# Kernel tuning notes

Hardware: AMD Instinct MI355X
Metric: run time of the kernel (lower is better)

## Reference

```python
import jax, jax.numpy as jnp
from jax import lax
import numpy as np

BLOCKS = 6
DIM = 768
D_STATE = 16
D_CONV = 4
EXPAND = 2
HEADDIM = 64
D_INNER = EXPAND * DIM              # 1536
NHEADS = D_INNER // HEADDIM        # 24
CONV_DIM = D_INNER + 2 * D_STATE   # 1568 (ngroups=1)
D_IN_PROJ = 2 * D_INNER + 2 * D_STATE + NHEADS  # 3128
NPITCH = 128


def setup_inputs() -> dict:
    key = jax.random.key(0)
    ks = jax.random.split(key, 16)
    B, L = 4, 4096
    s = 0.02
    return {
        "x": jax.random.normal(ks[0], (B, L, DIM), jnp.float32),
        "type_IDs": jax.random.randint(ks[1], (B, L), 0, 2),
        "in_proj_w": jax.random.normal(ks[2], (BLOCKS, D_IN_PROJ, DIM), jnp.float32) * s,
        "conv_w": jax.random.normal(ks[3], (BLOCKS, CONV_DIM, D_CONV), jnp.float32) * 0.1,
        "conv_b": jnp.zeros((BLOCKS, CONV_DIM), jnp.float32),
        "dt_bias": jax.random.uniform(ks[4], (BLOCKS, NHEADS), jnp.float32, -4.0, -2.0),
        "A_log": jnp.tile(jnp.log(jnp.linspace(1.0, 16.0, NHEADS, dtype=jnp.float32)), (BLOCKS, 1)),
        "D": jnp.ones((BLOCKS, NHEADS), jnp.float32),
        "norm_w": jnp.ones((BLOCKS, D_INNER), jnp.float32),
        "out_proj_w": jax.random.normal(ks[5], (BLOCKS, DIM, D_INNER), jnp.float32) * s,
        "head_w": jax.random.normal(ks[6], (2, DIM, DIM), jnp.float32) * s,
        "head_b": jnp.zeros((2, DIM), jnp.float32),
        "head_out_w": jax.random.normal(ks[7], (2, 4, NPITCH, DIM), jnp.float32) * s,
        "head_out_b": jnp.zeros((2, 4, NPITCH), jnp.float32),
    }


def _mamba2_block(x, Wi, cw, cb, dtb, Alog, Dp, nw, Wo):
    B, L, _ = x.shape
    zxbcdt = jnp.einsum('bld,ed->ble', x, Wi)                 # [B,L,D_IN_PROJ]
    z = zxbcdt[..., :D_INNER]
    xBC = zxbcdt[..., D_INNER:D_INNER + CONV_DIM]
    dt = zxbcdt[..., -NHEADS:]
    # causal depthwise conv1d over time
    xc = jnp.pad(jnp.swapaxes(xBC, 1, 2), ((0, 0), (0, 0), (D_CONV - 1, 0)))
    xBC = lax.conv_general_dilated(xc, cw[:, None, :], (1,), 'VALID',
                                   feature_group_count=CONV_DIM,
                                   dimension_numbers=('NCH', 'OIH', 'NCH'))
    xBC = jax.nn.silu(jnp.swapaxes(xBC, 1, 2) + cb)            # [B,L,CONV_DIM]
    xs = xBC[..., :D_INNER].reshape(B, L, NHEADS, HEADDIM)
    Bm = xBC[..., D_INNER:D_INNER + D_STATE]                   # [B,L,N]
    Cm = xBC[..., D_INNER + D_STATE:]                          # [B,L,N]
    dt = jax.nn.softplus(dt + dtb)                             # [B,L,H]
    dA = jnp.exp(dt * (-jnp.exp(Alog)))                        # [B,L,H]
    dtx = dt[..., None] * xs                                   # [B,L,H,P]

    def step(h, inp):
        dA_t, dtx_t, B_t, C_t = inp
        h = h * dA_t[:, :, None, None] + dtx_t[..., None] * B_t[:, None, None, :]
        y = jnp.einsum('bhpn,bn->bhp', h, C_t)
        return h, y

    h0 = jnp.zeros((B, NHEADS, HEADDIM, D_STATE), x.dtype)
    mv = lambda a: jnp.moveaxis(a, 1, 0)
    _, ys = lax.scan(step, h0, (mv(dA), mv(dtx), mv(Bm), mv(Cm)))
    y = jnp.moveaxis(ys, 0, 1) + Dp[None, None, :, None] * xs   # [B,L,H,P]
    y = y.reshape(B, L, D_INNER) * jax.nn.silu(z)               # gated
    y = y * lax.rsqrt(jnp.mean(y * y, -1, keepdims=True) + 1e-5) * nw
    return jnp.einsum('bli,di->bld', y, Wo)


def _head(t, hw, hb, ow, ob):
    h = jnp.einsum('bld,ed->ble', t, hw) + hb
    velocity = jnp.einsum('bld,pd->blp', h, ow[0]) + ob[0]
    onset = jax.nn.sigmoid(jnp.einsum('bld,pd->blp', h, ow[1]) + ob[1])
    offset = jax.nn.sigmoid(jnp.einsum('bld,pd->blp', h, ow[2]) + ob[2])
    frames = jax.nn.sigmoid(jnp.einsum('bld,pd->blp', h, ow[3]) + ob[3])
    return velocity, frames, onset, offset


def reference(x, type_IDs, in_proj_w, conv_w, conv_b, dt_bias, A_log, D,
              norm_w, out_proj_w, head_w, head_b, head_out_w, head_out_b):
    for i in range(BLOCKS):
        x = _mamba2_block(x, in_proj_w[i], conv_w[i], conv_b[i], dt_bias[i],
                          A_log[i], D[i], norm_w[i], out_proj_w[i])
    cmask = (type_IDs == 0).astype(x.dtype)[..., None]
    fmask = (type_IDs == 1).astype(x.dtype)[..., None]
    cv, cf, con, coff = _head(x, head_w[0], head_b[0], head_out_w[0], head_out_b[0])
    fv, ff, fon, foff = _head(x, head_w[1], head_b[1], head_out_w[1], head_out_b[1])
    # masked (instead of ragged boolean gather) to stay jit-compatible
    return jnp.stack([cv * cmask, cf * cmask, con * cmask, coff * cmask,
                      fv * fmask, ff * fmask, fon * fmask, foff * fmask])
```

## Files before the change

### kernel.cpp

```cpp
#include <hip/hip_runtime.h>
#include <cstdint>
#include <cstddef>

#define L_SEQ   4096
#define BATCH   4
#define DIMM    768
#define D_INNER 1536
#define NHEADS  24
#define HEADDIM 64
#define D_STATE 16
#define CONVD   1568
#define D_IPROJ 3128
#define ZXP     3200
#define SEGLEN  64
#define NSEG    (L_SEQ / SEGLEN)
#define BCP     44

typedef _Float16 f16x8 __attribute__((ext_vector_type(8)));
typedef _Float16 f16x4 __attribute__((ext_vector_type(4)));
typedef float    f32x4 __attribute__((ext_vector_type(4)));

__device__ __forceinline__ void glds16(const _Float16* g, _Float16* l) {
  __builtin_amdgcn_global_load_lds(
      (__attribute__((address_space(1))) unsigned int*)g,
      (__attribute__((address_space(3))) unsigned int*)l, 16, 0, 0);
}

__device__ __forceinline__ float fsilu(float x) {
  return x * __builtin_amdgcn_rcpf(1.f + __expf(-x));
}
__device__ __forceinline__ float fsig(float x) {
  return __builtin_amdgcn_rcpf(1.f + __expf(-x));
}

template <int OM>
__global__ __launch_bounds__(512, 1) void gemm256(
    const _Float16* __restrict__ A, long lda,
    const _Float16* __restrict__ W,
    const float* __restrict__ bias,
    _Float16* __restrict__ C, long ldc,
    int M, int N, int K)
{
  __shared__ __align__(16) _Float16 lds[65536];
  const int tid = threadIdx.x;
  const int lane = tid & 63, wid = tid >> 6;
  const int wm = wid >> 2, wn = wid & 3;
  const int la = lane & 15, lg = lane >> 4;
  const int srow = lane >> 3, schunk = lane & 7;

  const int nbx = gridDim.x, nby = gridDim.y;
  const int flat = blockIdx.y * nbx + blockIdx.x;
  const int xcd = flat & 7, idx = flat >> 3;
  const int rpx = nby >> 3;
  const long m0 = (long)(xcd * rpx + idx % rpx) * 256;
  const int n0 = (idx / rpx) * 256;

  const int nkt = K >> 6;

  auto stage = [&](int buf, int ht, int kt) {
#pragma unroll
    for (int p = 0; p < 2; ++p) {
      int rg = wid * 2 + p;
      int rl = (ht & 1) * 128 + rg * 8 + srow;
      int scn = schunk ^ (rl & 7);
      const _Float16* src;
      if (ht < 2) {
        src = A + (m0 + rl) * lda + kt * 64 + scn * 8;
      } else {
        int n = n0 + rl; if (n >= N) n = N - 1;
        src = W + (long)n * (long)K + kt * 64 + scn * 8;
      }
      _Float16* dst = lds + (ht >= 2 ? 32768 : 0) + buf * 16384
                          + ((ht & 1) * 128 + rg * 8) * 64;
      glds16(src, dst);
    }
  };

  f32x4 acc[8][4] = {};

  stage(0, 0, 0); stage(0, 1, 0); stage(0, 2, 0); stage(0, 3, 0);
  asm volatile("s_waitcnt vmcnt(0)" ::: "memory");
  __syncthreads();

  int buf = 0;
  for (int kt = 0; kt < nkt; ++kt) {
    const bool nl = (kt + 1 < nkt);
    const _Float16* Ab = lds + buf * 16384;
    const _Float16* Bb = lds + 32768 + buf * 16384;
    f16x8 bfr[4][2];
#pragma unroll
    for (int ph = 0; ph < 4; ++ph) {
      if (nl) stage(buf ^ 1, ph, kt + 1);
      if (ph == 0) {
#pragma unroll
        for (int j = 0; j < 4; ++j)
#pragma unroll
          for (int ks = 0; ks < 2; ++ks) {
            int rb = wn * 64 + j * 16 + la;
            int cc = ks * 4 + lg;
            bfr[j][ks] = *(const f16x8*)&Bb[rb * 64 + ((cc ^ (rb & 7)) << 3)];
          }
      }
      f16x8 af[2][2];
#pragma unroll
      for (int ii = 0; ii < 2; ++ii)
#pragma unroll
        for (int ks = 0; ks < 2; ++ks) {
          int ra = wm * 128 + (ph * 2 + ii) * 16 + la;
          int cc = ks * 4 + lg;
          af[ii][ks] = *(const f16x8*)&Ab[ra * 64 + ((cc ^ (ra & 7)) << 3)];
        }
      __builtin_amdgcn_s_setprio(1);
#pragma unroll
      for (int ii = 0; ii < 2; ++ii)
#pragma unroll
        for (int j = 0; j < 4; ++j)
#pragma unroll
          for (int ks = 0; ks < 2; ++ks)
            acc[ph * 2 + ii][j] = __builtin_amdgcn_mfma_f32_16x16x32_f16(
                af[ii][ks], bfr[j][ks], acc[ph * 2 + ii][j], 0, 0, 0);
      __builtin_amdgcn_s_setprio(0);
      if (ph == 3 && nl) asm volatile("s_waitcnt vmcnt(0)" ::: "memory");
      __syncthreads();
    }
    buf ^= 1;
  }

  _Float16* ep = lds + wid * 8192;
#pragma unroll
  for (int i = 0; i < 8; ++i)
#pragma unroll
    for (int j = 0; j < 4; ++j) {
      float bs = 0.f;
      if (OM == 2) bs = bias[n0 + wn * 64 + j * 16 + la];
#pragma unroll
      for (int r = 0; r < 4; ++r) {
        int row = i * 16 + lg * 4 + r;
        int jj = j ^ (row & 3);
        ep[row * 64 + jj * 16 + la] = (_Float16)(acc[i][j][r] + bs);
      }
    }
  asm volatile("s_waitcnt lgkmcnt(0)" ::: "memory");
#pragma unroll
  for (int it = 0; it < 16; ++it) {
    int row = it * 8 + (lane >> 3);
    int hc = lane & 7;
    int jj = (hc >> 1) ^ (row & 3);
    f16x8 v = *(const f16x8*)&ep[row * 64 + jj * 16 + (hc & 1) * 8];
    int gcol = n0 + wn * 64 + hc * 8;
    long grow = m0 + wm * 128 + row;
    if (gcol < N)
      *(f16x8*)&C[grow * ldc + gcol] = v;
  }
}

template <int OM>
__global__ __launch_bounds__(256, 2) void gemm_mfma(
    const _Float16* __restrict__ A, int lda,
    const _Float16* __restrict__ W,
    const float* __restrict__ bias,
    void* __restrict__ Cv, long ldc, long extra,
    int M, int N, int K,
    const int* __restrict__ tidsp, int thead)
{
  __shared__ __align__(16) char smem[33792];
  _Float16* As = (_Float16*)smem;
  _Float16* Ws = (_Float16*)(smem + 16384);
  const int tid = threadIdx.x;
  const int lane = tid & 63, wid = tid >> 6;
  const int wr = wid >> 1, wc = wid & 1;

  const int nbx = gridDim.x, nby = gridDim.y;
  const int flat = blockIdx.y * nbx + blockIdx.x;
  const int xcd = flat & 7;
  const int bidx = flat >> 3;
  const int rpx = nby >> 3;
  const int rl = bidx % rpx;
  const int ct = bidx / rpx;
  const long m0 = (long)(xcd * rpx + rl) * 128;
  const int n0 = ct * 128;

  const int la = lane & 15, lg = lane >> 4;
  const int srow = lane >> 3, schunk = lane & 7;

  f32x4 acc[4][4] = {};

  for (int k0 = 0; k0 < K; k0 += 64) {
    __syncthreads();
#pragma unroll
    for (int p = 0; p < 4; ++p) {
      const int rg = (wid << 2) + p;
      const int row = (rg << 3) + srow;
      const int scn = schunk ^ (row & 7);
      glds16(A + (m0 + row) * (long)lda + k0 + scn * 8, As + rg * 512);
      int n = n0 + row; if (n >= N) n = N - 1;
      glds16(W + (long)n * K + k0 + scn * 8, Ws + rg * 512);
    }
    asm volatile("s_waitcnt vmcnt(0)" ::: "memory");
    __syncthreads();
#pragma unroll
    for (int ks = 0; ks < 2; ++ks) {
      const int cc = ks * 4 + lg;
      f16x8 af[4], bfr[4];
#pragma unroll
      for (int i = 0; i < 4; ++i) {
        int ra = wr * 64 + i * 16 + la;
        int rb = wc * 64 + i * 16 + la;
        af[i]  = *(const f16x8*)&As[ra * 64 + ((cc ^ (ra & 7)) << 3)];
        bfr[i] = *(const f16x8*)&Ws[rb * 64 + ((cc ^ (rb & 7)) << 3)];
      }
#pragma unroll
      for (int i = 0; i < 4; ++i)
#pragma unroll
        for (int j = 0; j < 4; ++j)
          acc[i][j] = __builtin_amdgcn_mfma_f32_16x16x32_f16(af[i], bfr[j], acc[i][j], 0, 0, 0);
    }
  }

  float* epi = (float*)smem;
#pragma unroll
  for (int ph = 0; ph < 2; ++ph) {
    __syncthreads();
    if (wr == ph) {
#pragma unroll
      for (int i = 0; i < 4; ++i)
#pragma unroll
        for (int j = 0; j < 4; ++j)
#pragma unroll
          for (int r = 0; r < 4; ++r)
            epi[(i * 16 + lg * 4 + r) * 132 + wc * 64 + j * 16 + la] = acc[i][j][r];
    }
    __syncthreads();
    if (OM == 3) {
      const int q = n0 >> 7;
      const int rr = tid >> 5;
      const int ch = tid & 31;
#pragma unroll
      for (int ps = 0; ps < 8; ++ps) {
        int lrow = ps * 8 + rr;
        long gr = m0 + ph * 64 + lrow;
        float keep = (tidsp[gr] == thead) ? 1.f : 0.f;
        float4 v = *(float4*)&epi[lrow * 132 + ch * 4];
        float o[4] = {v.x, v.y, v.z, v.w};
#pragma unroll
        for (int e = 0; e < 4; ++e) {
          float vv = o[e] + bias[n0 + ch * 4 + e];
          if (q != 0) vv = fsig(vv);
          o[e] = vv * keep;
        }
        *(float4*)((float*)Cv + (long)q * extra + gr * 128 + ch * 4) =
            make_float4(o[0], o[1], o[2], o[3]);
      }
    }
  }
}

__global__ __launch_bounds__(256) void cvt_kernel(
    const float* __restrict__ src, _Float16* __restrict__ dst, long n4)
{
  long i = (long)blockIdx.x * 256 + threadIdx.x;
  long stride = (long)gridDim.x * 256;
  for (; i < n4; i += stride) {
    float4 v = *(const float4*)(src + i * 4);
    f16x4 o = { (_Float16)v.x, (_Float16)v.y, (_Float16)v.z, (_Float16)v.w };
    *(f16x4*)(dst + i * 4) = o;
  }
}

__global__ __launch_bounds__(256) void pack_head_kernel(
    const float* __restrict__ how, const float* __restrict__ hob,
    _Float16* __restrict__ howb, float* __restrict__ hobp)
{
  const int wmap[4] = {0, 3, 1, 2};
  int idx = blockIdx.x * 256 + threadIdx.x;
  if (idx < 2 * 512 * 768) {
    int t = idx / (512 * 768);
    int rem = idx - t * 512 * 768;
    int q = rem / (128 * 768);
    int rem2 = rem - q * 128 * 768;
    howb[idx] = (_Float16)how[((size_t)(t * 4 + wmap[q])) * 128 * 768 + rem2];
  }
  if (idx < 1024) {
    int t = idx >> 9, rem = idx & 511;
    int q = rem >> 7, pp = rem & 127;
    hobp[idx] = hob[(t * 4 + wmap[q]) * 128 + pp];
  }
}

__global__ __launch_bounds__(64) void ssdA_kernel(
    const _Float16* __restrict__ zx, const float* __restrict__ cw,
    const float* __restrict__ cb, const float* __restrict__ dtb,
    const float* __restrict__ alog, const float* __restrict__ Dv,
    _Float16* __restrict__ ybuf, _Float16* __restrict__ bcbuf,
    float* __restrict__ Hseg, float* __restrict__ cumq)
{
  __shared__ __align__(16) char sm[14848];
  _Float16* XV    = (_Float16*)sm;
  _Float16* bcraw = (_Float16*)sm;
  _Float16* BC    = (_Float16*)(sm + 8448);
  float* sa  = (float*)(sm + 14080);
  float* sdt = (float*)(sm + 14336);
  float* sws = (float*)(sm + 14592);
  const int lane = threadIdx.x;
  const int seg = blockIdx.x & (NSEG - 1);
  const int bh = blockIdx.x >> 6;
  const int h = bh % NHEADS, b = bh / NHEADS;
  const int bl0 = b * L_SEQ + seg * SEGLEN;
  const float LOG2E = 1.44269504088896f;

  for (int i = lane; i < 67 * 4; i += 64) {
    int r = i >> 2, q = (i & 3) << 3;
    f16x8 v = {};
    if (seg > 0 || r >= 3)
      v = *(const f16x8*)&zx[(size_t)(bl0 - 3 + r) * ZXP + 2 * D_INNER + q];
    *(f16x8*)&bcraw[r * 32 + q] = v;
  }
  {
    float raw = (float)zx[(size_t)(bl0 + lane) * ZXP + (D_INNER + CONVD) + h] + dtb[h];
    float sp = (raw > 20.f) ? raw : log1pf(__expf(raw));
    sdt[lane] = sp;
    float av = __expf(alog[h]) * sp * LOG2E;
#pragma unroll
    for (int off = 1; off < 64; off <<= 1) {
      float tv = __shfl_up(av, off, 64);
      if (lane >= off) av += tv;
    }
    sa[lane] = av;
    cumq[(size_t)bh * L_SEQ + seg * SEGLEN + lane] = exp2f(-av);
    float alast = __shfl(av, 63, 64);
    sws[lane] = exp2f(av - alast) * sp;
  }
  __syncthreads();

  for (int i = lane; i < SEGLEN * 32; i += 64) {
    int t = i >> 5, c = i & 31;
    float acc = cb[D_INNER + c];
#pragma unroll
    for (int k = 0; k < 4; ++k)
      acc = fmaf(cw[(D_INNER + c) * 4 + k], (float)bcraw[(t + k) * 32 + c], acc);
    _Float16 sh = (_Float16)fsilu(acc);
    BC[t * BCP + c] = sh;
    bcbuf[(size_t)(bl0 + t) * 32 + c] = sh;
  }
  __syncthreads();

  const int xch = h * HEADDIM + lane;
  const _Float16* xg = zx + (size_t)bl0 * ZXP + D_INNER + xch;
  const float cwx0 = cw[xch * 4 + 0], cwx1 = cw[xch * 4 + 1];
  const float cwx2 = cw[xch * 4 + 2], cwx3 = cw[xch * 4 + 3];
  const float cbx = cb[xch];
  float xw0 = 0.f, xw1 = 0.f, xw2 = 0.f;
  if (seg > 0) {
    xw0 = (float)xg[-3 * (long)ZXP];
    xw1 = (float)xg[-2 * (long)ZXP];
    xw2 = (float)xg[-1 * (long)ZXP];
  }
  float xcur = (float)xg[0];
  for (int t = 0; t < SEGLEN; ++t) {
    float xnext = (t < SEGLEN - 1) ? (float)xg[(size_t)(t + 1) * ZXP] : 0.f;
    float xa = cbx;
    xa = fmaf(cwx0, xw0, xa);
    xa = fmaf(cwx1, xw1, xa);
    xa = fmaf(cwx2, xw2, xa);
    xa = fmaf(cwx3, xcur, xa);
    XV[t * 66 + lane] = (_Float16)fsilu(xa);
    xw0 = xw1; xw1 = xw2; xw2 = xcur; xcur = xnext;
  }
  __syncthreads();

  const int la = lane & 15, lg = lane >> 4;

  f16x4 Mfrag[4][4];
  {
    f16x4 cf[4];
    float sat[4];
#pragma unroll
    for (int tt = 0; tt < 4; ++tt) {
      cf[tt] = *(const f16x4*)&BC[(tt * 16 + la) * BCP + 16 + lg * 4];
      sat[tt] = sa[tt * 16 + la];
    }
#pragma unroll
    for (int st = 0; st < 4; ++st) {
      f16x4 bfA = *(const f16x4*)&BC[(st * 16 + la) * BCP + lg * 4];
#pragma unroll
      for (int tt = 0; tt < 4; ++tt) {
        f32x4 a1 = {};
        a1 = __builtin_amdgcn_mfma_f32_16x16x16f16(bfA, cf[tt], a1, 0, 0, 0);
        f16x4 m;
#pragma unroll
        for (int r = 0; r < 4; ++r) {
          int s = st * 16 + lg * 4 + r;
          int t = tt * 16 + la;
          float mv = 0.f;
          if (s <= t) mv = a1[r] * exp2f(sa[s] - sat[tt]);
          m[r] = (_Float16)mv;
        }
        Mfrag[st][tt] = m;
      }
    }
  }

  f16x4 b3[4];
#pragma unroll
  for (int st = 0; st < 4; ++st) {
    f16x4 v;
#pragma unroll
    for (int e = 0; e < 4; ++e)
      v[e] = BC[(st * 16 + lg * 4 + e) * BCP + la];
    b3[st] = v;
  }

  const float Dh = Dv[h];
  float* Hst = Hseg + ((size_t)bh * NSEG + seg) * 1024;
#pragma unroll
  for (int pt = 0; pt < 4; ++pt) {
    f16x4 bf[4], af3[4];
#pragma unroll
    for (int st = 0; st < 4; ++st) {
      f16x4 v, w;
#pragma unroll
      for (int e = 0; e < 4; ++e) {
        int s = st * 16 + lg * 4 + e;
        float xv = (float)XV[s * 66 + pt * 16 + la];
        v[e] = (_Float16)(xv * sdt[s]);
        w[e] = (_Float16)(xv * sws[s]);
      }
      bf[st] = v; af3[st] = w;
    }
#pragma unroll
    for (int tt = 0; tt < 4; ++tt) {
      f32x4 a2 = {};
#pragma unroll
      for (int st = 0; st < 4; ++st)
        a2 = __builtin_amdgcn_mfma_f32_16x16x16f16(Mfrag[st][tt], bf[st], a2, 0, 0, 0);
#pragma unroll
      for (int r = 0; r < 4; ++r) {
        int t = tt * 16 + lg * 4 + r, p = pt * 16 + la;
        float y = a2[r] + Dh * (float)XV[t * 66 + p];
        ybuf[(size_t)(bl0 + t) * D_INNER + h * HEADDIM + p] = (_Float16)y;
      }
    }
    f32x4 a3 = {};
#pragma unroll
    for (int st = 0; st < 4; ++st)
      a3 = __builtin_amdgcn_mfma_f32_16x16x16f16(af3[st], b3[st], a3, 0, 0, 0);
#pragma unroll
    for (int r = 0; r < 4; ++r) {
      int p = pt * 16 + lg * 4 + r;
      Hst[p * 16 + la] = a3[r];
    }
  }
}

__global__ __launch_bounds__(1024) void scanB_kernel(
    float* __restrict__ Hseg, const float* __restrict__ cumq)
{
  const int bh = blockIdx.x;
  const int t = threadIdx.x;
  __shared__ float sp[NSEG];
  if (t < NSEG) sp[t] = cumq[(size_t)bh * L_SEQ + t * SEGLEN + (SEGLEN - 1)];
  __syncthreads();
  float v[NSEG];
#pragma unroll
  for (int s = 0; s < NSEG; ++s)
    v[s] = Hseg[((size_t)bh * NSEG + s) * 1024 + t];
  float h = 0.f;
#pragma unroll
  for (int s = 0; s < NSEG; ++s) {
    Hseg[((size_t)bh * NSEG + s) * 1024 + t] = h;
    h = fmaf(sp[s], h, v[s]);
  }
}

__global__ __launch_bounds__(64) void ssdC_kernel(
    _Float16* __restrict__ ybuf, const _Float16* __restrict__ bcbuf,
    const float* __restrict__ Hseg, const float* __restrict__ cumq)
{
  const int seg = blockIdx.x & (NSEG - 1);
  if (seg == 0) return;
  const int lane = threadIdx.x;
  const int bh = blockIdx.x >> 6;
  const int h = bh % NHEADS, b = bh / NHEADS;
  const int bl0 = b * L_SEQ + seg * SEGLEN;
  __shared__ float scq[SEGLEN];
  scq[lane] = cumq[(size_t)bh * L_SEQ + seg * SEGLEN + lane];
  const int la = lane & 15, lg = lane >> 4;
  const float* slot = Hseg + ((size_t)bh * NSEG + seg) * 1024;

  f16x8 a4[4], w4[4];
#pragma unroll
  for (int i = 0; i < 4; ++i) {
    f16x8 v = {};
    if (lg < 2)
      v = *(const f16x8*)&bcbuf[(size_t)(bl0 + i * 16 + la) * 32 + 16 + lg * 8];
    a4[i] = v;
  }
#pragma unroll
  for (int j = 0; j < 4; ++j) {
    f16x8 v = {};
    if (lg < 2) {
#pragma unroll
      for (int e = 0; e < 8; ++e)
        v[e] = (_Float16)slot[(j * 16 + la) * 16 + lg * 8 + e];
    }
    w4[j] = v;
  }
  f32x4 acc[4][4] = {};
#pragma unroll
  for (int i = 0; i < 4; ++i)
#pragma unroll
    for (int j = 0; j < 4; ++j)
      acc[i][j] = __builtin_amdgcn_mfma_f32_16x16x32_f16(a4[i], w4[j], acc[i][j], 0, 0, 0);
  __syncthreads();
#pragma unroll
  for (int i = 0; i < 4; ++i)
#pragma unroll
    for (int j = 0; j < 4; ++j)
#pragma unroll
      for (int r = 0; r < 4; ++r) {
        int t = i * 16 + lg * 4 + r, p = j * 16 + la;
        size_t ad = (size_t)(bl0 + t) * D_INNER + h * HEADDIM + p;
        ybuf[ad] = (_Float16)((float)ybuf[ad] + scq[t] * acc[i][j][r]);
      }
}

__global__ __launch_bounds__(256) void norm_kernel(
    const _Float16* __restrict__ y, _Float16* __restrict__ zx,
    const float* __restrict__ nw)
{
  const int row = blockIdx.x;
  const int tid = threadIdx.x;
  const _Float16* yr = y + (size_t)row * D_INNER;
  _Float16* zr = zx + (size_t)row * ZXP;
  float v[6];
  float ss = 0.f;
#pragma unroll
  for (int jj = 0; jj < 6; ++jj) {
    int c = jj * 256 + tid;
    float yv = (float)yr[c];
    float zv = (float)zr[c];
    float val = yv * fsilu(zv);
    v[jj] = val;
    ss = fmaf(val, val, ss);
  }
#pragma unroll
  for (int off = 32; off > 0; off >>= 1) ss += __shfl_xor(ss, off, 64);
  __shared__ float red[4];
  if ((tid & 63) == 0) red[tid >> 6] = ss;
  __syncthreads();
  float tot = red[0] + red[1] + red[2] + red[3];
  float rs = rsqrtf(tot * (1.f / 1536.f) + 1e-5f);
#pragma unroll
  for (int jj = 0; jj < 6; ++jj) {
    int c = jj * 256 + tid;
    zr[c] = (_Float16)(v[jj] * rs * nw[c]);
  }
}

extern "C" void kernel_launch(void* const* d_in, const int* in_sizes, int n_in,
                              void* d_out, int out_size, void* d_ws, size_t ws_size,
                              hipStream_t stream)
{
  const float* x_in = (const float*)d_in[0];
  const int*   tids = (const int*)d_in[1];
  const float* ipw  = (const float*)d_in[2];
  const float* cw   = (const float*)d_in[3];
  const float* cb   = (const float*)d_in[4];
  const float* dtb  = (const float*)d_in[5];
  const float* alog = (const float*)d_in[6];
  const float* Dv   = (const float*)d_in[7];
  const float* nw   = (const float*)d_in[8];
  const float* opw  = (const float*)d_in[9];
  const float* hw   = (const float*)d_in[10];
  const float* hb   = (const float*)d_in[11];
  const float* how  = (const float*)d_in[12];
  const float* hob  = (const float*)d_in[13];
  float* out = (float*)d_out;

  char* p = (char*)d_ws;
  _Float16* ipw_b = (_Float16*)p; p += (size_t)14413824 * 2;
  _Float16* opw_b = (_Float16*)p; p += (size_t)7077888 * 2;
  _Float16* hw_b  = (_Float16*)p; p += (size_t)1179648 * 2;
  _Float16* how_b = (_Float16*)p; p += (size_t)786432 * 2;
  float*    hob_p = (float*)p;    p += (size_t)1024 * 4;
  const size_t used_w = (size_t)(p - (char*)d_ws);
  const size_t PB = 54528000;
  int nb = 4;
  while (nb > 1 && used_w + (size_t)nb * PB > ws_size) nb >>= 1;

  cvt_kernel<<<8192, 256, 0, stream>>>(ipw, ipw_b, 14413824 / 4);
  cvt_kernel<<<6912, 256, 0, stream>>>(opw, opw_b, 7077888 / 4);
  cvt_kernel<<<1152, 256, 0, stream>>>(hw, hw_b, 1179648 / 4);
  pack_head_kernel<<<3072, 256, 0, stream>>>(how, hob, how_b, hob_p);

  for (int b0 = 0; b0 < BATCH; b0 += nb) {
    const int MT = nb * L_SEQ;
    _Float16* zx    = (_Float16*)p;
    _Float16* ybuf  = zx + (size_t)MT * ZXP;
    _Float16* bcbuf = ybuf + (size_t)MT * D_INNER;
    float*    Hseg  = (float*)(bcbuf + (size_t)MT * 32);
    float*    cumq  = Hseg + (size_t)nb * NHEADS * NSEG * 1024;
    _Float16* xbuf  = (_Float16*)(cumq + (size_t)MT * NHEADS);
    _Float16* hbuf  = zx;

    cvt_kernel<<<6144, 256, 0, stream>>>(x_in + (size_t)b0 * L_SEQ * DIMM,
                                         xbuf, (long)MT * DIMM / 4);

    for (int i = 0; i < 6; ++i) {
      gemm256<0><<<dim3(13, MT / 256), 512, 0, stream>>>(
          xbuf, DIMM, ipw_b + (size_t)i * D_IPROJ * DIMM, nullptr,
          zx, ZXP, MT, D_IPROJ, DIMM);
      ssdA_kernel<<<nb * NHEADS * NSEG, 64, 0, stream>>>(
          zx, cw + (size_t)i * CONVD * 4, cb + i * CONVD,
          dtb + i * NHEADS, alog + i * NHEADS, Dv + i * NHEADS,
          ybuf, bcbuf, Hseg, cumq);
      scanB_kernel<<<nb * NHEADS, 1024, 0, stream>>>(Hseg, cumq);
      ssdC_kernel<<<nb * NHEADS * NSEG, 64, 0, stream>>>(ybuf, bcbuf, Hseg, cumq);
      norm_kernel<<<MT, 256, 0, stream>>>(ybuf, zx, nw + i * D_INNER);
      gemm256<0><<<dim3(3, MT / 256), 512, 0, stream>>>(
          zx, ZXP, opw_b + (size_t)i * DIMM * D_INNER, nullptr,
          xbuf, DIMM, MT, DIMM, D_INNER);
    }

    for (int t = 0; t < 2; ++t) {
      gemm256<2><<<dim3(3, MT / 256), 512, 0, stream>>>(
          xbuf, DIMM, hw_b + (size_t)t * DIMM * DIMM, hb + t * DIMM,
          hbuf, DIMM, MT, DIMM, DIMM);
      gemm_mfma<3><<<dim3(4, MT / 128), 256, 0, stream>>>(
          hbuf, DIMM, how_b + (size_t)t * 512 * DIMM, hob_p + t * 512,
          out + (size_t)t * 4 * 16384 * 128 + (size_t)b0 * L_SEQ * 128,
          128, (long)16384 * 128, MT, 512, DIMM,
          tids + (size_t)b0 * L_SEQ, t);
    }
  }
}
```

Measured before the change: 2.041 ms.

## Restructure gemm256 main loop: single barrier per k-tile, bulk prefetch

Replaces the four-phase inner loop, which issued part of the next tile's global-to-LDS load and a __syncthreads in every phase, with one up-front prefetch of the whole next tile followed by all 8x4x2 MFMAs and a single s_barrier per k-tile. The LDS layout is reorganised so A and B tiles of one buffer sit together, and each wave loads a matching slice. The epilogue swizzle changes to an 8-way XOR on column chunks, with a sched_barrier added. This cuts barrier count and synchronisation stalls, at the cost of less interleaving of loads with compute and possibly higher register pressure.

Measured after the change: 1.867 ms. 8.5% less time.

```diff
diff --git a/kernel.cpp b/kernel.cpp
--- a/kernel.cpp
+++ b/kernel.cpp
@@ -47,6 +47,9 @@
   const int wm = wid >> 2, wn = wid & 3;
   const int la = lane & 15, lg = lane >> 4;
   const int srow = lane >> 3, schunk = lane & 7;
+  const int ga = wid & 3;
+  const int hb = wn >> 1;
+  const int gb = (wm << 1) | (wn & 1);
 
   const int nbx = gridDim.x, nby = gridDim.y;
   const int flat = blockIdx.y * nbx + blockIdx.x;
@@ -54,103 +57,92 @@
   const int rpx = nby >> 3;
   const long m0 = (long)(xcd * rpx + idx % rpx) * 256;
   const int n0 = (idx / rpx) * 256;
-
   const int nkt = K >> 6;
 
-  auto stage = [&](int buf, int ht, int kt) {
-#pragma unroll
-    for (int p = 0; p < 2; ++p) {
-      int rg = wid * 2 + p;
-      int rl = (ht & 1) * 128 + rg * 8 + srow;
-      int scn = schunk ^ (rl & 7);
-      const _Float16* src;
-      if (ht < 2) {
-        src = A + (m0 + rl) * lda + kt * 64 + scn * 8;
-      } else {
-        int n = n0 + rl; if (n >= N) n = N - 1;
-        src = W + (long)n * (long)K + kt * 64 + scn * 8;
-      }
-      _Float16* dst = lds + (ht >= 2 ? 32768 : 0) + buf * 16384
-                          + ((ht & 1) * 128 + rg * 8) * 64;
-      glds16(src, dst);
+  auto stage = [&](int buf, int kt) {
+    _Float16* Ab = lds + buf * 32768;
+    _Float16* Bb = lds + buf * 32768 + 16384;
+#pragma unroll
+    for (int q = 0; q < 4; ++q) {
+      int rla = wm * 128 + (ga * 4 + q) * 8;
+      int row = rla + srow;
+      int scn = schunk ^ (row & 7);
+      glds16(A + (m0 + row) * lda + kt * 64 + scn * 8, Ab + rla * 64);
+      int rlb = hb * 128 + (gb * 4 + q) * 8;
+      int rowb = rlb + srow;
+      int n = n0 + rowb; if (n >= N) n = N - 1;
+      int scnb = schunk ^ (rowb & 7);
+      glds16(W + (long)n * (long)K + kt * 64 + scnb * 8, Bb + rlb * 64);
     }
   };
 
   f32x4 acc[8][4] = {};
 
-  stage(0, 0, 0); stage(0, 1, 0); stage(0, 2, 0); stage(0, 3, 0);
+  stage(0, 0);
   asm volatile("s_waitcnt vmcnt(0)" ::: "memory");
-  __syncthreads();
+  __builtin_amdgcn_s_barrier();
 
   int buf = 0;
   for (int kt = 0; kt < nkt; ++kt) {
-    const bool nl = (kt + 1 < nkt);
-    const _Float16* Ab = lds + buf * 16384;
-    const _Float16* Bb = lds + 32768 + buf * 16384;
+    if (kt + 1 < nkt) stage(buf ^ 1, kt + 1);
+    const _Float16* Ab = lds + buf * 32768;
+    const _Float16* Bb = lds + buf * 32768 + 16384;
     f16x8 bfr[4][2];
 #pragma unroll
-    for (int ph = 0; ph < 4; ++ph) {
-      if (nl) stage(buf ^ 1, ph, kt + 1);
-      if (ph == 0) {
-#pragma unroll
-        for (int j = 0; j < 4; ++j)
-#pragma unroll
-          for (int ks = 0; ks < 2; ++ks) {
-            int rb = wn * 64 + j * 16 + la;
-            int cc = ks * 4 + lg;
-            bfr[j][ks] = *(const f16x8*)&Bb[rb * 64 + ((cc ^ (rb & 7)) << 3)];
-          }
-      }
-      f16x8 af[2][2];
-#pragma unroll
-      for (int ii = 0; ii < 2; ++ii)
-#pragma unroll
-        for (int ks = 0; ks < 2; ++ks) {
-          int ra = wm * 128 + (ph * 2 + ii) * 16 + la;
-          int cc = ks * 4 + lg;
-          af[ii][ks] = *(const f16x8*)&Ab[ra * 64 + ((cc ^ (ra & 7)) << 3)];
-        }
+    for (int j = 0; j < 4; ++j)
+#pragma unroll
+      for (int ks = 0; ks < 2; ++ks) {
+        int rb = wn * 64 + j * 16 + la;
+        int cc = ks * 4 + lg;
+        bfr[j][ks] = *(const f16x8*)&Bb[rb * 64 + ((cc ^ (rb & 7)) << 3)];
+      }
+#pragma unroll
+    for (int m = 0; m < 8; ++m) {
+      f16x8 am[2];
+#pragma unroll
+      for (int ks = 0; ks < 2; ++ks) {
+        int ra = wm * 128 + m * 16 + la;
+        int cc = ks * 4 + lg;
+        am[ks] = *(const f16x8*)&Ab[ra * 64 + ((cc ^ (ra & 7)) << 3)];
+      }
       __builtin_amdgcn_s_setprio(1);
 #pragma unroll
-      for (int ii = 0; ii < 2; ++ii)
-#pragma unroll
-        for (int j = 0; j < 4; ++j)
-#pragma unroll
-          for (int ks = 0; ks < 2; ++ks)
-            acc[ph * 2 + ii][j] = __builtin_amdgcn_mfma_f32_16x16x32_f16(
-                af[ii][ks], bfr[j][ks], acc[ph * 2 + ii][j], 0, 0, 0);
+      for (int j = 0; j < 4; ++j)
+#pragma unroll
+        for (int ks = 0; ks < 2; ++ks)
+          acc[m][j] = __builtin_amdgcn_mfma_f32_16x16x32_f16(
+              am[ks], bfr[j][ks], acc[m][j], 0, 0, 0);
       __builtin_amdgcn_s_setprio(0);
-      if (ph == 3 && nl) asm volatile("s_waitcnt vmcnt(0)" ::: "memory");
-      __syncthreads();
-    }
+    }
+    if (kt + 1 < nkt) asm volatile("s_waitcnt vmcnt(0)" ::: "memory");
+    __builtin_amdgcn_s_barrier();
     buf ^= 1;
   }
 
   _Float16* ep = lds + wid * 8192;
 #pragma unroll
-  for (int i = 0; i < 8; ++i)
+  for (int m = 0; m < 8; ++m)
 #pragma unroll
     for (int j = 0; j < 4; ++j) {
       float bs = 0.f;
       if (OM == 2) bs = bias[n0 + wn * 64 + j * 16 + la];
 #pragma unroll
       for (int r = 0; r < 4; ++r) {
-        int row = i * 16 + lg * 4 + r;
-        int jj = j ^ (row & 3);
-        ep[row * 64 + jj * 16 + la] = (_Float16)(acc[i][j][r] + bs);
+        int row = m * 16 + lg * 4 + r;
+        int c = j * 16 + la;
+        ep[row * 64 + (c ^ ((row & 7) << 3))] = (_Float16)(acc[m][j][r] + bs);
       }
     }
   asm volatile("s_waitcnt lgkmcnt(0)" ::: "memory");
+  __builtin_amdgcn_sched_barrier(0);
 #pragma unroll
   for (int it = 0; it < 16; ++it) {
     int row = it * 8 + (lane >> 3);
-    int hc = lane & 7;
-    int jj = (hc >> 1) ^ (row & 3);
-    f16x8 v = *(const f16x8*)&ep[row * 64 + jj * 16 + (hc & 1) * 8];
-    int gcol = n0 + wn * 64 + hc * 8;
+    int c0 = (lane & 7) * 8;
+    f16x8 v = *(const f16x8*)&ep[row * 64 + (c0 ^ ((row & 7) << 3))];
     long grow = m0 + wm * 128 + row;
-    if (gcol < N)
-      *(f16x8*)&C[grow * ldc + gcol] = v;
+    int gcol = n0 + wn * 64 + c0;
+    if (gcol < N) *(f16x8*)&C[grow * ldc + gcol] = v;
   }
 }
 
```
